# Performance work log

Measured on AMD Instinct MI355X. Metric: run time of the kernel, lower is better.

The kernel has to match this reference:

```python
import jax, jax.numpy as jnp
import numpy as np

E1, E2, E3, M, DEC_H, OUT = 512, 512, 512, 1024, 2048, 1000
B = 16384

def _linear_params(key, fan_in, fan_out):
    kw, kb = jax.random.split(key)
    bound = 1.0 / np.sqrt(fan_in)
    W = jax.random.uniform(kw, (fan_out, fan_in), jnp.float32, -bound, bound)
    b = jax.random.uniform(kb, (fan_out,), jnp.float32, -bound, bound)
    return W, b

def setup_inputs() -> dict:
    key = jax.random.key(0)
    ks = jax.random.split(key, 7)
    tube = jax.random.normal(ks[0], (B, E1 + E2 + E3), jnp.float32)
    w1_W, w1_b = _linear_params(ks[1], E1, M)
    w2_W, w2_b = _linear_params(ks[2], E2, M)
    w3_W, w3_b = _linear_params(ks[3], E3, M)
    wh_W, wh_b = _linear_params(ks[4], 3 * M, M)
    wd1_W, wd1_b = _linear_params(ks[5], 2 * M, DEC_H)
    wd2_W, wd2_b = _linear_params(ks[6], DEC_H, OUT)
    return dict(tube=tube, w1_W=w1_W, w1_b=w1_b, w2_W=w2_W, w2_b=w2_b,
                w3_W=w3_W, w3_b=w3_b, wh_W=wh_W, wh_b=wh_b,
                wd1_W=wd1_W, wd1_b=wd1_b, wd2_W=wd2_W, wd2_b=wd2_b)

def reference(tube, w1_W, w1_b, w2_W, w2_b, w3_W, w3_b, wh_W, wh_b,
              wd1_W, wd1_b, wd2_W, wd2_b):
    relu = jax.nn.relu
    x1 = tube[:, :E1]
    x2 = tube[:, E1:E1 + E2]
    x3 = tube[:, E1 + E2:E1 + E2 + E3]
    P1 = relu(x1 @ w1_W.T + w1_b)   # [B, M]
    P2 = relu(x2 @ w2_W.T + w2_b)
    P3 = relu(x3 @ w3_W.T + w3_b)
    hid1 = jnp.concatenate([P1, P2, P3], axis=1)      # [B, 3M]
    last_hid = relu(hid1 @ wh_W.T + wh_b)             # [B, M]
    # diag(matmul(last_hid, P.T)) == row-wise dot product
    alpha1 = jnp.sum(last_hid * P1, axis=1)
    alpha2 = jnp.sum(last_hid * P2, axis=1)
    alpha3 = jnp.sum(last_hid * P3, axis=1)
    alphas = jnp.stack([alpha1, alpha2, alpha3], axis=1)  # [B, 3]
    weights = jax.nn.softmax(alphas, axis=1)
    context = (weights[:, 0:1] * P1 + weights[:, 1:2] * P2
               + weights[:, 2:3] * P3)                   # [B, M]
    decode_start = jnp.concatenate([context, last_hid], axis=1)  # [B, 2M]
    out = relu(decode_start @ wd1_W.T + wd1_b)
    out = out @ wd2_W.T + wd2_b                           # [B, OUT]
    return out
```

## Files before the change

### kernel.cpp

```cpp
#include <hip/hip_runtime.h>
#include <hip/hip_bf16.h>


typedef __bf16 bf16_t;
typedef __bf16 bf16x4 __attribute__((ext_vector_type(4)));
typedef __bf16 bf16x8 __attribute__((ext_vector_type(8)));
typedef float  f32x4  __attribute__((ext_vector_type(4)));
typedef float  f32x16 __attribute__((ext_vector_type(16)));

#define AS1(p) (const __attribute__((address_space(1))) void*)(p)
#define AS3(p) (__attribute__((address_space(3))) void*)(p)

__global__ void cvt_f32_bf16_v4(const float* __restrict__ src, bf16_t* __restrict__ dst,
                                int n4src, int n4tot) {
  for (int i = blockIdx.x * blockDim.x + threadIdx.x; i < n4tot; i += gridDim.x * blockDim.x) {
    bf16x4 o;
    if (i < n4src) {
      float4 f = ((const float4*)src)[i];
      o[0] = (bf16_t)f.x; o[1] = (bf16_t)f.y; o[2] = (bf16_t)f.z; o[3] = (bf16_t)f.w;
    } else {
      o[0] = (bf16_t)0.0f; o[1] = (bf16_t)0.0f; o[2] = (bf16_t)0.0f; o[3] = (bf16_t)0.0f;
    }
    *(bf16x4*)(dst + (size_t)i * 4) = o;
  }
}

__global__ void cvt_weights(const float* __restrict__ w1, const float* __restrict__ w2,
                            const float* __restrict__ w3, const float* __restrict__ wh,
                            const float* __restrict__ wd1, const float* __restrict__ wd2,
                            bf16_t* __restrict__ w123, bf16_t* __restrict__ whB,
                            bf16_t* __restrict__ wd1B, bf16_t* __restrict__ wd2B) {
  const int stride = gridDim.x * blockDim.x;
  for (int i = blockIdx.x * blockDim.x + threadIdx.x; i < 2752512; i += stride) {
    const float* s; bf16_t* d; int o; int ns = 1 << 30;
    if (i < 131072)       { s = w1;  d = w123;           o = i; }
    else if (i < 262144)  { s = w2;  d = w123 + 524288;  o = i - 131072; }
    else if (i < 393216)  { s = w3;  d = w123 + 1048576; o = i - 262144; }
    else if (i < 1179648) { s = wh;  d = whB;            o = i - 393216; }
    else if (i < 2228224) { s = wd1; d = wd1B;           o = i - 1179648; }
    else                  { s = wd2; d = wd2B;           o = i - 2228224; ns = 512000; }
    bf16x4 v;
    if (o < ns) {
      float4 f = ((const float4*)s)[o];
      v[0] = (bf16_t)f.x; v[1] = (bf16_t)f.y; v[2] = (bf16_t)f.z; v[3] = (bf16_t)f.w;
    } else {
      v[0] = (bf16_t)0.0f; v[1] = (bf16_t)0.0f; v[2] = (bf16_t)0.0f; v[3] = (bf16_t)0.0f;
    }
    *(bf16x4*)(d + (size_t)o * 4) = v;
  }
}

__global__ void concat_bias3(const float* __restrict__ a, const float* __restrict__ b,
                             const float* __restrict__ c, float* __restrict__ dst) {
  int i = blockIdx.x * blockDim.x + threadIdx.x;
  if (i < 1024) dst[i] = a[i];
  else if (i < 2048) dst[i] = b[i - 1024];
  else if (i < 3072) dst[i] = c[i - 2048];
}

template<bool BDIAG, bool RELU, bool OUT_BF16>
__global__ __launch_bounds__(512, 2)
void gemm256(const bf16_t* __restrict__ A, int lda,
             const bf16_t* __restrict__ Bw, int ldb,
             const float* __restrict__ bias,
             void* __restrict__ Cout, int ldc,
             int K, int Nmask, int nbx)
{
  extern __shared__ char lds[];
  bf16_t* Ab = (bf16_t*)lds;
  bf16_t* Bb = (bf16_t*)(lds + 65536);

  const int t   = threadIdx.x;
  const int ln  = t & 63;
  const int w   = t >> 6;
  const int l31 = ln & 31, lk = ln >> 5;
  const int wm  = w >> 2, wn = w & 3;

  const int nb = (int)gridDim.x;
  const int id = (int)blockIdx.x;
  const int id_sw = (id & 7) * (nb >> 3) + (id >> 3);
  const int bx = id_sw % nbx, by = id_sw / nbx;
  const int rowBase = by * 256;
  const int colBase = bx * 256;
  const int aCol0 = BDIAG ? (colBase >> 10) * 512 : 0;

  const int srow = (w << 4) + (ln >> 2);
  const int scol = (((ln & 3) ^ (ln >> 3)) & 3) << 3;

  const bf16_t* aS = A  + (size_t)(rowBase + srow) * lda + aCol0 + scol;
  const bf16_t* bS = Bw + (size_t)(colBase + srow) * ldb + scol;
  const size_t aI = (size_t)128 * lda;
  const size_t bI = (size_t)128 * ldb;
  bf16_t* daW = Ab + (w << 9);
  bf16_t* dbW = Bb + (w << 9);

  const int key = (l31 >> 1) & 3;
  const int g0e = ((lk ^ key) << 3);
  const int aRow = (wm * 128 + l31) * 32;
  const int bRow = (wn * 64  + l31) * 32;

  const int nt = K >> 5;

  f32x16 acc[4][2] = {};

  #define STAGE(kt, s)                                                              \
    do {                                                                            \
      const bf16_t* a_ = aS + (size_t)(kt) * 32;                                    \
      const bf16_t* b_ = bS + (size_t)(kt) * 32;                                    \
      bf16_t* da_ = daW + (s) * 8192;                                               \
      bf16_t* db_ = dbW + (s) * 8192;                                               \
      __builtin_amdgcn_global_load_lds(AS1(a_),      AS3(da_),        16, 0, 0);    \
      __builtin_amdgcn_global_load_lds(AS1(a_ + aI), AS3(da_ + 4096), 16, 0, 0);    \
      __builtin_amdgcn_global_load_lds(AS1(b_),      AS3(db_),        16, 0, 0);    \
      __builtin_amdgcn_global_load_lds(AS1(b_ + bI), AS3(db_ + 4096), 16, 0, 0);    \
    } while (0)

  STAGE(0, 0); STAGE(1, 1); STAGE(2, 2);
  asm volatile("s_waitcnt vmcnt(8)" ::: "memory");
  __builtin_amdgcn_s_barrier();
  asm volatile("" ::: "memory");

  for (int j = 0; j < nt; ++j) {
    const int s = j & 3;
    const bf16_t* As_ = Ab + s * 8192;
    const bf16_t* Bs_ = Bb + s * 8192;

    bf16x8 aR[4][2], bR[2][2];
    #pragma unroll
    for (int mf = 0; mf < 4; ++mf) {
      aR[mf][0] = *(const bf16x8*)(As_ + aRow + mf * 1024 + g0e);
      aR[mf][1] = *(const bf16x8*)(As_ + aRow + mf * 1024 + (g0e ^ 16));
    }
    #pragma unroll
    for (int nf = 0; nf < 2; ++nf) {
      bR[nf][0] = *(const bf16x8*)(Bs_ + bRow + nf * 1024 + g0e);
      bR[nf][1] = *(const bf16x8*)(Bs_ + bRow + nf * 1024 + (g0e ^ 16));
    }

    if (j + 3 < nt) {
      STAGE(j + 3, ((j + 3) & 3));
      asm volatile("s_waitcnt vmcnt(8)" ::: "memory");
    } else if (j + 2 < nt) {
      asm volatile("s_waitcnt vmcnt(4)" ::: "memory");
    } else if (j + 1 < nt) {
      asm volatile("s_waitcnt vmcnt(0)" ::: "memory");
    }
    asm volatile("s_waitcnt lgkmcnt(0)" ::: "memory");
    __builtin_amdgcn_s_barrier();
    asm volatile("" ::: "memory");

    __builtin_amdgcn_s_setprio(1);
    #pragma unroll
    for (int ks = 0; ks < 2; ++ks)
      #pragma unroll
      for (int mf = 0; mf < 4; ++mf)
        #pragma unroll
        for (int nf = 0; nf < 2; ++nf)
          acc[mf][nf] = __builtin_amdgcn_mfma_f32_32x32x16_bf16(
              aR[mf][ks], bR[nf][ks], acc[mf][nf], 0, 0, 0);
    __builtin_amdgcn_s_setprio(0);
  }
  #undef STAGE

  #pragma unroll
  for (int mf = 0; mf < 4; ++mf) {
    #pragma unroll
    for (int nf = 0; nf < 2; ++nf) {
      const int col = colBase + wn * 64 + nf * 32 + l31;
      const float bv = (col < Nmask) ? bias[col] : 0.0f;
      #pragma unroll
      for (int reg = 0; reg < 16; ++reg) {
        const int row = rowBase + wm * 128 + mf * 32 + (reg & 3) + 8 * (reg >> 2) + 4 * lk;
        float v = acc[mf][nf][reg] + bv;
        if (RELU) v = fmaxf(v, 0.0f);
        if (OUT_BF16) {
          ((bf16_t*)Cout)[(size_t)row * ldc + col] = (bf16_t)v;
        } else {
          if (col < Nmask) ((float*)Cout)[(size_t)row * ldc + col] = v;
        }
      }
    }
  }
}

__global__ __launch_bounds__(256)
void attn_ctx(const bf16_t* __restrict__ P, bf16_t* __restrict__ ds) {
  __shared__ float red[3][4];
  __shared__ float wsh[3];
  const int r = blockIdx.x;
  const int t = threadIdx.x;
  const bf16_t* Prow = P + (size_t)r * 3072;
  bf16_t* dsrow = ds + (size_t)r * 2048;

  const int j = t * 4;
  bf16x4 lv = *(const bf16x4*)(dsrow + 1024 + j);
  float lhv[4], pv[3][4];
  float s[3] = {0.f, 0.f, 0.f};
  #pragma unroll
  for (int q = 0; q < 4; q++) lhv[q] = (float)lv[q];
  #pragma unroll
  for (int e = 0; e < 3; e++) {
    bf16x4 p = *(const bf16x4*)(Prow + e * 1024 + j);
    #pragma unroll
    for (int q = 0; q < 4; q++) {
      pv[e][q] = (float)p[q];
      s[e] += lhv[q] * pv[e][q];
    }
  }
  #pragma unroll
  for (int off = 32; off > 0; off >>= 1) {
    #pragma unroll
    for (int e = 0; e < 3; e++) s[e] += __shfl_down(s[e], off, 64);
  }
  const int w = t >> 6, l = t & 63;
  if (l == 0) {
    #pragma unroll
    for (int e = 0; e < 3; e++) red[e][w] = s[e];
  }
  __syncthreads();
  if (t == 0) {
    float a0 = red[0][0] + red[0][1] + red[0][2] + red[0][3];
    float a1 = red[1][0] + red[1][1] + red[1][2] + red[1][3];
    float a2 = red[2][0] + red[2][1] + red[2][2] + red[2][3];
    float mx = fmaxf(a0, fmaxf(a1, a2));
    float e0 = expf(a0 - mx), e1 = expf(a1 - mx), e2 = expf(a2 - mx);
    float inv = 1.0f / (e0 + e1 + e2);
    wsh[0] = e0 * inv; wsh[1] = e1 * inv; wsh[2] = e2 * inv;
  }
  __syncthreads();
  const float w0 = wsh[0], w1 = wsh[1], w2 = wsh[2];
  bf16x4 o;
  #pragma unroll
  for (int q = 0; q < 4; q++)
    o[q] = (bf16_t)(w0 * pv[0][q] + w1 * pv[1][q] + w2 * pv[2][q]);
  *(bf16x4*)(dsrow + j) = o;
}

extern "C" void kernel_launch(void* const* d_in, const int* in_sizes, int n_in,
                              void* d_out, int out_size, void* d_ws, size_t ws_size,
                              hipStream_t stream) {
  (void)in_sizes; (void)n_in; (void)out_size; (void)ws_size;

  const float* tube = (const float*)d_in[0];
  const float* w1W  = (const float*)d_in[1];
  const float* w1b  = (const float*)d_in[2];
  const float* w2W  = (const float*)d_in[3];
  const float* w2b  = (const float*)d_in[4];
  const float* w3W  = (const float*)d_in[5];
  const float* w3b  = (const float*)d_in[6];
  const float* whW  = (const float*)d_in[7];
  const float* whb  = (const float*)d_in[8];
  const float* wd1W = (const float*)d_in[9];
  const float* wd1b = (const float*)d_in[10];
  const float* wd2W = (const float*)d_in[11];
  const float* wd2b = (const float*)d_in[12];

  char* ws = (char*)d_ws;
  bf16_t* P       = (bf16_t*)(ws + 0);
  bf16_t* ds      = (bf16_t*)(ws + 100663296);
  bf16_t* wd1B    = (bf16_t*)(ws + 167772160);
  bf16_t* wd2B    = (bf16_t*)(ws + 176160768);
  bf16_t* whB     = (bf16_t*)(ws + 180355072);
  bf16_t* w123B   = (bf16_t*)(ws + 186646528);
  bf16_t* tubeB   = (bf16_t*)(ws + 189792256);
  bf16_t* out1    = (bf16_t*)(ws + 180355072);
  float*  bias123 = (float*)(ws + 247463936);

  hipFuncSetAttribute((const void*)(gemm256<true,  true,  true >),
                      hipFuncAttributeMaxDynamicSharedMemorySize, 131072);
  hipFuncSetAttribute((const void*)(gemm256<false, true,  true >),
                      hipFuncAttributeMaxDynamicSharedMemorySize, 131072);
  hipFuncSetAttribute((const void*)(gemm256<false, false, false>),
                      hipFuncAttributeMaxDynamicSharedMemorySize, 131072);

  hipLaunchKernelGGL(cvt_f32_bf16_v4, dim3(2048), dim3(256), 0, stream,
                     tube, tubeB, 6291456, 6291456);
  hipLaunchKernelGGL(cvt_weights, dim3(2048), dim3(256), 0, stream,
                     w1W, w2W, w3W, whW, wd1W, wd2W, w123B, whB, wd1B, wd2B);
  hipLaunchKernelGGL(concat_bias3, dim3(12), dim3(256), 0, stream, w1b, w2b, w3b, bias123);

  hipLaunchKernelGGL((gemm256<true, true, true>), dim3(12 * 64), dim3(512), 131072, stream,
                     tubeB, 1536, w123B, 512, bias123, (void*)P, 3072, 512, 3072, 12);
  hipLaunchKernelGGL((gemm256<false, true, true>), dim3(4 * 64), dim3(512), 131072, stream,
                     P, 3072, whB, 3072, whb, (void*)(ds + 1024), 2048, 3072, 1024, 4);
  hipLaunchKernelGGL(attn_ctx, dim3(16384), dim3(256), 0, stream, P, ds);
  hipLaunchKernelGGL((gemm256<false, true, true>), dim3(8 * 64), dim3(512), 131072, stream,
                     ds, 2048, wd1B, 2048, wd1b, (void*)out1, 2048, 2048, 2048, 8);
  hipLaunchKernelGGL((gemm256<false, false, false>), dim3(4 * 64), dim3(512), 131072, stream,
                     out1, 2048, wd2B, 2048, wd2b, d_out, 1000, 2048, 1000, 4);
}
```

Before: 429.8 us.

## Load GEMM B operand directly from global into registers, halving LDS

The B (weight) tile no longer goes through LDS. Each wave loads its B fragments straight from global memory into registers, double-buffered across two k-steps, while A stays staged in LDS. The MFMA shape changes from 32x32x16 to 16x16x32 with an 8x4 accumulator grid, and dynamic LDS drops from 128KB to 64KB. This removes LDS traffic and capacity for B, but waves that share columns now issue redundant global loads, and each k-step now drains vmcnt(0) fully before its barrier.

```diff
diff --git a/kernel.cpp b/kernel.cpp
--- a/kernel.cpp
+++ b/kernel.cpp
@@ -6,7 +6,6 @@
 typedef __bf16 bf16x4 __attribute__((ext_vector_type(4)));
 typedef __bf16 bf16x8 __attribute__((ext_vector_type(8)));
 typedef float  f32x4  __attribute__((ext_vector_type(4)));
-typedef float  f32x16 __attribute__((ext_vector_type(16)));
 
 #define AS1(p) (const __attribute__((address_space(1))) void*)(p)
 #define AS3(p) (__attribute__((address_space(3))) void*)(p)
@@ -68,12 +67,11 @@
 {
   extern __shared__ char lds[];
   bf16_t* Ab = (bf16_t*)lds;
-  bf16_t* Bb = (bf16_t*)(lds + 65536);
 
   const int t   = threadIdx.x;
   const int ln  = t & 63;
   const int w   = t >> 6;
-  const int l31 = ln & 31, lk = ln >> 5;
+  const int l15 = ln & 15, lhi = ln >> 4;
   const int wm  = w >> 2, wn = w & 3;
 
   const int nb = (int)gridDim.x;
@@ -86,97 +84,107 @@
 
   const int srow = (w << 4) + (ln >> 2);
   const int scol = (((ln & 3) ^ (ln >> 3)) & 3) << 3;
-
-  const bf16_t* aS = A  + (size_t)(rowBase + srow) * lda + aCol0 + scol;
-  const bf16_t* bS = Bw + (size_t)(colBase + srow) * ldb + scol;
+  const bf16_t* aS = A + (size_t)(rowBase + srow) * lda + aCol0 + scol;
   const size_t aI = (size_t)128 * lda;
-  const size_t bI = (size_t)128 * ldb;
   bf16_t* daW = Ab + (w << 9);
-  bf16_t* dbW = Bb + (w << 9);
-
-  const int key = (l31 >> 1) & 3;
-  const int g0e = ((lk ^ key) << 3);
-  const int aRow = (wm * 128 + l31) * 32;
-  const int bRow = (wn * 64  + l31) * 32;
+
+  const int key  = (l15 >> 1) & 3;
+  const int fcol = (lhi ^ key) << 3;
+  const int aOff = (wm * 128 + l15) * 32 + fcol;
+
+  const bf16_t* bP = Bw + (size_t)(colBase + wn * 64 + l15) * ldb + lhi * 8;
+  const size_t bNf = (size_t)16 * ldb;
 
   const int nt = K >> 5;
 
-  f32x16 acc[4][2] = {};
-
-  #define STAGE(kt, s)                                                              \
+  f32x4 acc[8][4] = {};
+  bf16x8 bE[4], bO[4];
+
+  #define STAGE_A(kt, s)                                                            \
     do {                                                                            \
       const bf16_t* a_ = aS + (size_t)(kt) * 32;                                    \
-      const bf16_t* b_ = bS + (size_t)(kt) * 32;                                    \
       bf16_t* da_ = daW + (s) * 8192;                                               \
-      bf16_t* db_ = dbW + (s) * 8192;                                               \
       __builtin_amdgcn_global_load_lds(AS1(a_),      AS3(da_),        16, 0, 0);    \
       __builtin_amdgcn_global_load_lds(AS1(a_ + aI), AS3(da_ + 4096), 16, 0, 0);    \
-      __builtin_amdgcn_global_load_lds(AS1(b_),      AS3(db_),        16, 0, 0);    \
-      __builtin_amdgcn_global_load_lds(AS1(b_ + bI), AS3(db_ + 4096), 16, 0, 0);    \
-    } while (0)
-
-  STAGE(0, 0); STAGE(1, 1); STAGE(2, 2);
-  asm volatile("s_waitcnt vmcnt(8)" ::: "memory");
-  __builtin_amdgcn_s_barrier();
-  asm volatile("" ::: "memory");
-
-  for (int j = 0; j < nt; ++j) {
-    const int s = j & 3;
-    const bf16_t* As_ = Ab + s * 8192;
-    const bf16_t* Bs_ = Bb + s * 8192;
-
-    bf16x8 aR[4][2], bR[2][2];
-    #pragma unroll
-    for (int mf = 0; mf < 4; ++mf) {
-      aR[mf][0] = *(const bf16x8*)(As_ + aRow + mf * 1024 + g0e);
-      aR[mf][1] = *(const bf16x8*)(As_ + aRow + mf * 1024 + (g0e ^ 16));
-    }
-    #pragma unroll
-    for (int nf = 0; nf < 2; ++nf) {
-      bR[nf][0] = *(const bf16x8*)(Bs_ + bRow + nf * 1024 + g0e);
-      bR[nf][1] = *(const bf16x8*)(Bs_ + bRow + nf * 1024 + (g0e ^ 16));
-    }
-
-    if (j + 3 < nt) {
-      STAGE(j + 3, ((j + 3) & 3));
-      asm volatile("s_waitcnt vmcnt(8)" ::: "memory");
-    } else if (j + 2 < nt) {
-      asm volatile("s_waitcnt vmcnt(4)" ::: "memory");
-    } else if (j + 1 < nt) {
-      asm volatile("s_waitcnt vmcnt(0)" ::: "memory");
-    }
-    asm volatile("s_waitcnt lgkmcnt(0)" ::: "memory");
-    __builtin_amdgcn_s_barrier();
-    asm volatile("" ::: "memory");
-
-    __builtin_amdgcn_s_setprio(1);
-    #pragma unroll
-    for (int ks = 0; ks < 2; ++ks)
+    } while (0)
+
+  #define LOADB(kt, BR)                                                             \
+    do {                                                                            \
+      const bf16_t* p_ = bP + (size_t)(kt) * 32;                                    \
+      BR[0] = *(const bf16x8*)(p_);                                                 \
+      BR[1] = *(const bf16x8*)(p_ + bNf);                                           \
+      BR[2] = *(const bf16x8*)(p_ + 2 * bNf);                                       \
+      BR[3] = *(const bf16x8*)(p_ + 3 * bNf);                                       \
+    } while (0)
+
+  #define MFMAC(AF, BR)                                                             \
+    do {                                                                            \
+      __builtin_amdgcn_s_setprio(1);                                                \
+      _Pragma("unroll")                                                             \
+      for (int mf_ = 0; mf_ < 8; ++mf_)                                             \
+        _Pragma("unroll")                                                           \
+        for (int nf_ = 0; nf_ < 4; ++nf_)                                           \
+          acc[mf_][nf_] = __builtin_amdgcn_mfma_f32_16x16x32_bf16(                  \
+              AF[mf_], BR[nf_], acc[mf_][nf_], 0, 0, 0);                            \
+      __builtin_amdgcn_s_setprio(0);                                                \
+    } while (0)
+
+  #define DRAIN_BAR()                                                               \
+    do {                                                                            \
+      asm volatile("s_waitcnt vmcnt(0)" ::: "memory");                              \
+      asm volatile("s_waitcnt lgkmcnt(0)" ::: "memory");                            \
+      __builtin_amdgcn_s_barrier();                                                 \
+      asm volatile("" ::: "memory");                                                \
+    } while (0)
+
+  STAGE_A(0, 0); STAGE_A(1, 1); STAGE_A(2, 2);
+  LOADB(0, bE);
+  DRAIN_BAR();
+
+  for (int j = 0; j < nt; j += 2) {
+    {
+      const int s = j & 3;
+      const bf16_t* As_ = Ab + s * 8192 + aOff;
+      bf16x8 af[8];
       #pragma unroll
-      for (int mf = 0; mf < 4; ++mf)
-        #pragma unroll
-        for (int nf = 0; nf < 2; ++nf)
-          acc[mf][nf] = __builtin_amdgcn_mfma_f32_32x32x16_bf16(
-              aR[mf][ks], bR[nf][ks], acc[mf][nf], 0, 0, 0);
-    __builtin_amdgcn_s_setprio(0);
-  }
-  #undef STAGE
-
-  #pragma unroll
-  for (int mf = 0; mf < 4; ++mf) {
-    #pragma unroll
-    for (int nf = 0; nf < 2; ++nf) {
-      const int col = colBase + wn * 64 + nf * 32 + l31;
+      for (int mf = 0; mf < 8; ++mf) af[mf] = *(const bf16x8*)(As_ + mf * 512);
+      if (j + 3 < nt) STAGE_A(j + 3, ((j + 3) & 3));
+      LOADB(j + 1, bO);
+      MFMAC(af, bE);
+      DRAIN_BAR();
+    }
+    {
+      const int s = (j + 1) & 3;
+      const bf16_t* As_ = Ab + s * 8192 + aOff;
+      bf16x8 af[8];
+      #pragma unroll
+      for (int mf = 0; mf < 8; ++mf) af[mf] = *(const bf16x8*)(As_ + mf * 512);
+      if (j + 4 < nt) STAGE_A(j + 4, ((j + 4) & 3));
+      if (j + 2 < nt) LOADB(j + 2, bE);
+      MFMAC(af, bO);
+      if (j + 2 < nt) DRAIN_BAR();
+    }
+  }
+  #undef STAGE_A
+  #undef LOADB
+  #undef MFMAC
+  #undef DRAIN_BAR
+
+  #pragma unroll
+  for (int mf = 0; mf < 8; ++mf) {
+    const int row = rowBase + wm * 128 + mf * 16 + lhi * 4;
+    #pragma unroll
+    for (int nf = 0; nf < 4; ++nf) {
+      const int col = colBase + wn * 64 + nf * 16 + l15;
       const float bv = (col < Nmask) ? bias[col] : 0.0f;
       #pragma unroll
-      for (int reg = 0; reg < 16; ++reg) {
-        const int row = rowBase + wm * 128 + mf * 32 + (reg & 3) + 8 * (reg >> 2) + 4 * lk;
-        float v = acc[mf][nf][reg] + bv;
+      for (int i = 0; i < 4; ++i) {
+        float v = acc[mf][nf][i] + bv;
         if (RELU) v = fmaxf(v, 0.0f);
         if (OUT_BF16) {
-          ((bf16_t*)Cout)[(size_t)row * ldc + col] = (bf16_t)v;
+          ((bf16_t*)Cout)[(size_t)(row + i) * ldc + col] = (bf16_t)v;
         } else {
-          if (col < Nmask) ((float*)Cout)[(size_t)row * ldc + col] = v;
+          if (col < Nmask) ((float*)Cout)[(size_t)(row + i) * ldc + col] = v;
         }
       }
     }
@@ -267,11 +275,11 @@
   float*  bias123 = (float*)(ws + 247463936);
 
   hipFuncSetAttribute((const void*)(gemm256<true,  true,  true >),
-                      hipFuncAttributeMaxDynamicSharedMemorySize, 131072);
+                      hipFuncAttributeMaxDynamicSharedMemorySize, 65536);
   hipFuncSetAttribute((const void*)(gemm256<false, true,  true >),
-                      hipFuncAttributeMaxDynamicSharedMemorySize, 131072);
+                      hipFuncAttributeMaxDynamicSharedMemorySize, 65536);
   hipFuncSetAttribute((const void*)(gemm256<false, false, false>),
-                      hipFuncAttributeMaxDynamicSharedMemorySize, 131072);
+                      hipFuncAttributeMaxDynamicSharedMemorySize, 65536);
 
   hipLaunchKernelGGL(cvt_f32_bf16_v4, dim3(2048), dim3(256), 0, stream,
                      tube, tubeB, 6291456, 6291456);
@@ -279,13 +287,13 @@
                      w1W, w2W, w3W, whW, wd1W, wd2W, w123B, whB, wd1B, wd2B);
   hipLaunchKernelGGL(concat_bias3, dim3(12), dim3(256), 0, stream, w1b, w2b, w3b, bias123);
 
-  hipLaunchKernelGGL((gemm256<true, true, true>), dim3(12 * 64), dim3(512), 131072, stream,
+  hipLaunchKernelGGL((gemm256<true, true, true>), dim3(12 * 64), dim3(512), 65536, stream,
                      tubeB, 1536, w123B, 512, bias123, (void*)P, 3072, 512, 3072, 12);
-  hipLaunchKernelGGL((gemm256<false, true, true>), dim3(4 * 64), dim3(512), 131072, stream,
+  hipLaunchKernelGGL((gemm256<false, true, true>), dim3(4 * 64), dim3(512), 65536, stream,
                      P, 3072, whB, 3072, whb, (void*)(ds + 1024), 2048, 3072, 1024, 4);
   hipLaunchKernelGGL(attn_ctx, dim3(16384), dim3(256), 0, stream, P, ds);
-  hipLaunchKernelGGL((gemm256<false, true, true>), dim3(8 * 64), dim3(512), 131072, stream,
+  hipLaunchKernelGGL((gemm256<false, true, true>), dim3(8 * 64), dim3(512), 65536, stream,
                      ds, 2048, wd1B, 2048, wd1b, (void*)out1, 2048, 2048, 2048, 8);
-  hipLaunchKernelGGL((gemm256<false, false, false>), dim3(4 * 64), dim3(512), 131072, stream,
+  hipLaunchKernelGGL((gemm256<false, false, false>), dim3(4 * 64), dim3(512), 65536, stream,
                      out1, 2048, wd2B, 2048, wd2b, d_out, 1000, 2048, 1000, 4);
 }
```

After: 621.2 us. +44.5%, slower.
